# Kernel optimization log

Hardware: AMD Instinct MI355X
Metric: run time of the kernel (lower is better)

Reference implementation:

```python
import jax, jax.numpy as jnp
import numpy as np


def make_hadamard(n, seed=1):
    # Sylvester Hadamard matrix with random sign diagonal, orthonormalized.
    assert (n & (n - 1)) == 0, 'n must be a power of 2'
    H = np.array([[1.0]], dtype=np.float32)
    while H.shape[0] < n:
        H = np.block([[H, H], [H, -H]])
    rng = np.random.default_rng(seed)
    signs = rng.choice(np.array([-1.0, 1.0], dtype=np.float32), size=n)
    H = (H * signs[None, :]) / np.sqrt(n, dtype=np.float32)
    return jnp.asarray(H)


def setup_inputs() -> dict:
    key = jax.random.key(0)
    k_x, = jax.random.split(key, 1)
    B, S, D = 4, 4096, 2048
    x = jax.random.normal(k_x, (B, S, D), dtype=jnp.float32)
    scale = jnp.ones((1,), dtype=jnp.float32) * 0.1  # must be > 0
    hadamard = make_hadamard(D)
    return {
        'x': x,
        'scale': scale,
        'hadamard': hadamard,
        'Qn': 8,
        'Qp': 7,
        'num_elements': B * S * D,
    }


def reference(x, scale, hadamard, Qn, Qp, num_elements):
    # grad_scale_mode == 'LSQ_grad_scale'
    qn = float(Qn)
    qp = float(Qp)
    grad_scale = 1.0 / jnp.sqrt(jnp.float32(num_elements) * qp)
    # scale = (scale - scale*gs).detach() + scale*gs  (forward value unchanged)
    bw_scale = scale * grad_scale
    s = jax.lax.stop_gradient(scale - bw_scale) + bw_scale  # shape [1]

    x_rot = jnp.matmul(x, hadamard)           # [B,S,D]
    xq = jnp.clip(x_rot / s, -qn, qp)
    # straight-through rounding: (round(x)-x).detach() + x
    yq = jax.lax.stop_gradient(jnp.round(xq) - xq) + xq
    y = yq * s
    return jnp.matmul(y, hadamard.T)          # un-rotate
```

## Files before the change

kernel.cpp:

```cpp
#include <hip/hip_runtime.h>
#include <math.h>


constexpr int D  = 2048;
constexpr int NR = 8;

#define LGKM0() __asm__ __volatile__("s_waitcnt lgkmcnt(0)" ::: "memory")

__device__ __forceinline__ void bfly(float4& a, float4& b) {
    float4 ta = a, tb = b;
    a.x = ta.x + tb.x; a.y = ta.y + tb.y; a.z = ta.z + tb.z; a.w = ta.w + tb.w;
    b.x = ta.x - tb.x; b.y = ta.y - tb.y; b.z = ta.z - tb.z; b.w = ta.w - tb.w;
}

__device__ __forceinline__ void reg_stages(float4 (&v)[NR]) {
    #pragma unroll
    for (int m = 1; m <= 4; m <<= 1) {
        #pragma unroll
        for (int r = 0; r < NR; ++r)
            if ((r & m) == 0) bfly(v[r], v[r | m]);
    }
}

__device__ __forceinline__ void comp_stages(float4 (&v)[NR]) {
    #pragma unroll
    for (int r = 0; r < NR; ++r) {
        float a, b;
        a = v[r].x; b = v[r].y; v[r].x = a + b; v[r].y = a - b;
        a = v[r].z; b = v[r].w; v[r].z = a + b; v[r].w = a - b;
        a = v[r].x; b = v[r].z; v[r].x = a + b; v[r].z = a - b;
        a = v[r].y; b = v[r].w; v[r].y = a + b; v[r].w = a - b;
    }
}

__device__ __forceinline__ float quant1(float xh, float h0, float s, float inv_s,
                                        float nqn, float qp) {
    float u = xh * h0 * inv_s;
    u = fminf(fmaxf(u, nqn), qp);
    float q = rintf(u);
    return q * (s * h0);
}

__global__ __launch_bounds__(256) void lsq_fwht_kernel(
    const float* __restrict__ x,
    const float* __restrict__ scale,
    const float* __restrict__ hadamard,
    const int*   __restrict__ qn_p,
    const int*   __restrict__ qp_p,
    const int*   __restrict__ ne_p,
    float*       __restrict__ out,
    int rows)
{
    __shared__ float smem[4][D];

    const int lane = threadIdx.x & 63;
    const int wave = threadIdx.x >> 6;
    const int row  = blockIdx.x * 4 + wave;
    if (row >= rows) return;

    float* lds = smem[wave];
    const int llo = lane & 7;
    const int lhi = lane >> 3;

    const float sc    = scale[0];
    const float qp    = (float)qp_p[0];
    const float nqn   = -(float)qn_p[0];
    const float gs    = 1.0f / sqrtf((float)ne_p[0] * qp);
    const float bw    = sc * gs;
    const float s     = (sc - bw) + bw;
    const float inv_s = 1.0f / s;

    float4 v[NR];
    {
        const float4* x4 = reinterpret_cast<const float4*>(x + (size_t)row * D) + lane;
        #pragma unroll
        for (int r = 0; r < NR; ++r) v[r] = x4[(size_t)r * 64];
    }
    float4 h[NR];
    {
        const float4* h4 = reinterpret_cast<const float4*>(hadamard);
        #pragma unroll
        for (int r = 0; r < NR; ++r) h[r] = h4[lhi * 64 + r * 8 + llo];
    }

    const int wA  = (lane * 4) ^ (lhi << 2);
    const int rBb = lhi * 256 + llo * 32;
    const int rCb = lhi * 256 + ((llo * 4) ^ (lhi << 2));

    comp_stages(v);
    reg_stages(v);
    #pragma unroll
    for (int r = 0; r < NR; ++r)
        *reinterpret_cast<float4*>(lds + r * 256 + wA) = v[r];
    LGKM0();
    #pragma unroll
    for (int r = 0; r < NR; ++r)
        v[r] = *reinterpret_cast<const float4*>(lds + rBb + ((r * 4) ^ (llo << 2)));
    reg_stages(v);
    #pragma unroll
    for (int r = 0; r < NR; ++r)
        *reinterpret_cast<float4*>(lds + rBb + ((r * 4) ^ (lhi << 2))) = v[r];
    LGKM0();
    #pragma unroll
    for (int r = 0; r < NR; ++r)
        v[r] = *reinterpret_cast<const float4*>(lds + rCb + r * 32);
    reg_stages(v);

    #pragma unroll
    for (int r = 0; r < NR; ++r) {
        v[r].x = quant1(v[r].x, h[r].x, s, inv_s, nqn, qp);
        v[r].y = quant1(v[r].y, h[r].y, s, inv_s, nqn, qp);
        v[r].z = quant1(v[r].z, h[r].z, s, inv_s, nqn, qp);
        v[r].w = quant1(v[r].w, h[r].w, s, inv_s, nqn, qp);
    }

    reg_stages(v);
    #pragma unroll
    for (int r = 0; r < NR; ++r)
        *reinterpret_cast<float4*>(lds + rCb + r * 32) = v[r];
    LGKM0();
    #pragma unroll
    for (int r = 0; r < NR; ++r)
        v[r] = *reinterpret_cast<const float4*>(lds + rBb + ((r * 4) ^ (lhi << 2)));
    reg_stages(v);
    #pragma unroll
    for (int r = 0; r < NR; ++r)
        *reinterpret_cast<float4*>(lds + rBb + ((r * 4) ^ (llo << 2))) = v[r];
    LGKM0();
    #pragma unroll
    for (int r = 0; r < NR; ++r)
        v[r] = *reinterpret_cast<const float4*>(lds + r * 256 + wA);
    reg_stages(v);
    comp_stages(v);

    {
        float4* y4 = reinterpret_cast<float4*>(out + (size_t)row * D) + lane;
        #pragma unroll
        for (int r = 0; r < NR; ++r) y4[(size_t)r * 64] = v[r];
    }
}

extern "C" void kernel_launch(void* const* d_in, const int* in_sizes, int n_in,
                              void* d_out, int out_size, void* d_ws, size_t ws_size,
                              hipStream_t stream) {
    const float* x        = (const float*)d_in[0];
    const float* scale    = (const float*)d_in[1];
    const float* hadamard = (const float*)d_in[2];
    const int*   Qn       = (const int*)d_in[3];
    const int*   Qp       = (const int*)d_in[4];
    const int*   ne       = (const int*)d_in[5];
    float*       out      = (float*)d_out;

    const int rows = in_sizes[0] / D;
    const int grid = (rows + 3) / 4;

    lsq_fwht_kernel<<<grid, 256, 0, stream>>>(x, scale, hadamard, Qn, Qp, ne,
                                              out, rows);
}
```

Before: 247.2 us.

## Use persistent grid-stride rows with register prefetch of next row

Launches a fixed grid of 1024 blocks where each wave loops over rows with a grid stride. The next row's input is loaded into registers while the current row runs through the FWHT and quantization, so global loads overlap compute. The scale is also folded into the hadamard sign vector to save multiplies, the LDS swizzle addressing is simplified, and launch bounds now request occupancy 4. The cost is more register pressure from the prefetch buffer, which could lower occupancy or cause spills.

Result: slower. 314.7 us (+27.3%).

```diff
diff --git a/kernel.cpp b/kernel.cpp
--- a/kernel.cpp
+++ b/kernel.cpp
@@ -33,15 +33,14 @@
     }
 }
 
-__device__ __forceinline__ float quant1(float xh, float h0, float s, float inv_s,
+__device__ __forceinline__ float quant1(float xh, float hs, float inv_s2,
                                         float nqn, float qp) {
-    float u = xh * h0 * inv_s;
+    float u = xh * hs * inv_s2;
     u = fminf(fmaxf(u, nqn), qp);
-    float q = rintf(u);
-    return q * (s * h0);
+    return rintf(u) * hs;
 }
 
-__global__ __launch_bounds__(256) void lsq_fwht_kernel(
+__global__ __launch_bounds__(256, 4) void lsq_fwht_kernel(
     const float* __restrict__ x,
     const float* __restrict__ scale,
     const float* __restrict__ hadamard,
@@ -49,14 +48,14 @@
     const int*   __restrict__ qp_p,
     const int*   __restrict__ ne_p,
     float*       __restrict__ out,
-    int rows)
+    int rows, int stride)
 {
     __shared__ float smem[4][D];
 
     const int lane = threadIdx.x & 63;
     const int wave = threadIdx.x >> 6;
-    const int row  = blockIdx.x * 4 + wave;
-    if (row >= rows) return;
+    const int row0 = blockIdx.x * 4 + wave;
+    if (row0 >= rows) return;
 
     float* lds = smem[wave];
     const int llo = lane & 7;
@@ -69,74 +68,96 @@
     const float bw    = sc * gs;
     const float s     = (sc - bw) + bw;
     const float inv_s = 1.0f / s;
+    const float inv_s2 = inv_s * inv_s;
 
-    float4 v[NR];
-    {
-        const float4* x4 = reinterpret_cast<const float4*>(x + (size_t)row * D) + lane;
-        #pragma unroll
-        for (int r = 0; r < NR; ++r) v[r] = x4[(size_t)r * 64];
-    }
     float4 h[NR];
     {
         const float4* h4 = reinterpret_cast<const float4*>(hadamard);
         #pragma unroll
-        for (int r = 0; r < NR; ++r) h[r] = h4[lhi * 64 + r * 8 + llo];
+        for (int r = 0; r < NR; ++r) {
+            h[r] = h4[lhi * 64 + r * 8 + llo];
+            h[r].x *= s; h[r].y *= s; h[r].z *= s; h[r].w *= s;
+        }
     }
 
-    const int wA  = (lane * 4) ^ (lhi << 2);
-    const int rBb = lhi * 256 + llo * 32;
-    const int rCb = lhi * 256 + ((llo * 4) ^ (lhi << 2));
+    const int aA  = lhi * 32 + ((llo ^ lhi) << 2);
+    const int aBC = lhi * 256;
+    const int t2  = llo << 2;
 
-    comp_stages(v);
-    reg_stages(v);
-    #pragma unroll
-    for (int r = 0; r < NR; ++r)
-        *reinterpret_cast<float4*>(lds + r * 256 + wA) = v[r];
-    LGKM0();
-    #pragma unroll
-    for (int r = 0; r < NR; ++r)
-        v[r] = *reinterpret_cast<const float4*>(lds + rBb + ((r * 4) ^ (llo << 2)));
-    reg_stages(v);
-    #pragma unroll
-    for (int r = 0; r < NR; ++r)
-        *reinterpret_cast<float4*>(lds + rBb + ((r * 4) ^ (lhi << 2))) = v[r];
-    LGKM0();
-    #pragma unroll
-    for (int r = 0; r < NR; ++r)
-        v[r] = *reinterpret_cast<const float4*>(lds + rCb + r * 32);
-    reg_stages(v);
+    const float4* x4 = reinterpret_cast<const float4*>(x)   + lane;
+    float4*       y4 = reinterpret_cast<float4*>(out)       + lane;
 
-    #pragma unroll
-    for (int r = 0; r < NR; ++r) {
-        v[r].x = quant1(v[r].x, h[r].x, s, inv_s, nqn, qp);
-        v[r].y = quant1(v[r].y, h[r].y, s, inv_s, nqn, qp);
-        v[r].z = quant1(v[r].z, h[r].z, s, inv_s, nqn, qp);
-        v[r].w = quant1(v[r].w, h[r].w, s, inv_s, nqn, qp);
+    float4 v[NR], p[NR];
+    {
+        const float4* src = x4 + (size_t)row0 * (D / 4);
+        #pragma unroll
+        for (int r = 0; r < NR; ++r) v[r] = src[(size_t)r * 64];
     }
 
-    reg_stages(v);
-    #pragma unroll
-    for (int r = 0; r < NR; ++r)
-        *reinterpret_cast<float4*>(lds + rCb + r * 32) = v[r];
-    LGKM0();
-    #pragma unroll
-    for (int r = 0; r < NR; ++r)
-        v[r] = *reinterpret_cast<const float4*>(lds + rBb + ((r * 4) ^ (lhi << 2)));
-    reg_stages(v);
-    #pragma unroll
-    for (int r = 0; r < NR; ++r)
-        *reinterpret_cast<float4*>(lds + rBb + ((r * 4) ^ (llo << 2))) = v[r];
-    LGKM0();
-    #pragma unroll
-    for (int r = 0; r < NR; ++r)
-        v[r] = *reinterpret_cast<const float4*>(lds + r * 256 + wA);
-    reg_stages(v);
-    comp_stages(v);
+    for (int row = row0; row < rows; row += stride) {
+        const int nrow = row + stride;
+        if (nrow < rows) {
+            const float4* src = x4 + (size_t)nrow * (D / 4);
+            #pragma unroll
+            for (int r = 0; r < NR; ++r) p[r] = src[(size_t)r * 64];
+        }
 
-    {
-        float4* y4 = reinterpret_cast<float4*>(out + (size_t)row * D) + lane;
+        comp_stages(v);
+        reg_stages(v);
         #pragma unroll
-        for (int r = 0; r < NR; ++r) y4[(size_t)r * 64] = v[r];
+        for (int r = 0; r < NR; ++r)
+            *reinterpret_cast<float4*>(lds + r * 256 + aA) = v[r];
+        LGKM0();
+        #pragma unroll
+        for (int r = 0; r < NR; ++r)
+            v[r] = *reinterpret_cast<const float4*>(lds + aBC + llo * 32 + ((r << 2) ^ t2));
+        reg_stages(v);
+        #pragma unroll
+        for (int r = 0; r < NR; ++r)
+            *reinterpret_cast<float4*>(lds + aBC + llo * 32 + ((r << 2) ^ t2)) = v[r];
+        LGKM0();
+        #pragma unroll
+        for (int r = 0; r < NR; ++r)
+            v[r] = *reinterpret_cast<const float4*>(lds + aBC + r * 32 + ((r << 2) ^ t2));
+        reg_stages(v);
+
+        #pragma unroll
+        for (int r = 0; r < NR; ++r) {
+            v[r].x = quant1(v[r].x, h[r].x, inv_s2, nqn, qp);
+            v[r].y = quant1(v[r].y, h[r].y, inv_s2, nqn, qp);
+            v[r].z = quant1(v[r].z, h[r].z, inv_s2, nqn, qp);
+            v[r].w = quant1(v[r].w, h[r].w, inv_s2, nqn, qp);
+        }
+
+        reg_stages(v);
+        #pragma unroll
+        for (int r = 0; r < NR; ++r)
+            *reinterpret_cast<float4*>(lds + aBC + r * 32 + ((r << 2) ^ t2)) = v[r];
+        LGKM0();
+        #pragma unroll
+        for (int r = 0; r < NR; ++r)
+            v[r] = *reinterpret_cast<const float4*>(lds + aBC + llo * 32 + ((r << 2) ^ t2));
+        reg_stages(v);
+        #pragma unroll
+        for (int r = 0; r < NR; ++r)
+            *reinterpret_cast<float4*>(lds + aBC + llo * 32 + ((r << 2) ^ t2)) = v[r];
+        LGKM0();
+        #pragma unroll
+        for (int r = 0; r < NR; ++r)
+            v[r] = *reinterpret_cast<const float4*>(lds + r * 256 + aA);
+        reg_stages(v);
+        comp_stages(v);
+
+        {
+            float4* dst = y4 + (size_t)row * (D / 4);
+            #pragma unroll
+            for (int r = 0; r < NR; ++r) dst[(size_t)r * 64] = v[r];
+        }
+
+        if (nrow < rows) {
+            #pragma unroll
+            for (int r = 0; r < NR; ++r) v[r] = p[r];
+        }
     }
 }
 
@@ -152,8 +173,9 @@
     float*       out      = (float*)d_out;
 
     const int rows = in_sizes[0] / D;
-    const int grid = (rows + 3) / 4;
+    const int grid   = 1024;
+    const int stride = grid * 4;
 
     lsq_fwht_kernel<<<grid, 256, 0, stream>>>(x, scale, hadamard, Qn, Qp, ne,
-                                              out, rows);
+                                              out, rows, stride);
 }
```
